# Kernel tuning notes

Measured on AMD Instinct MI355X. Metric: run time of the kernel, lower is better.

The kernel has to match this reference:

```python
import jax, jax.numpy as jnp
import numpy as np
from jax import lax

DIVISOR = 2.0


def setup_inputs() -> dict:
    key = jax.random.key(0)
    k1, k2, k3, k4 = jax.random.split(key, 4)
    x = jax.random.normal(k1, (128, 8, 32, 32, 32), dtype=jnp.float32)
    conv_weight = jax.random.normal(k2, (16, 8, 3, 3, 3), dtype=jnp.float32) * 0.1
    conv_bias = jax.random.normal(k3, (16,), dtype=jnp.float32) * 0.1
    bias = jax.random.normal(k4, (16, 1, 1, 1), dtype=jnp.float32) * 0.1
    return {"x": x, "conv_weight": conv_weight, "conv_bias": conv_bias, "bias": bias}


def reference(x, conv_weight, conv_bias, bias):
    # Conv3d, stride 1, no padding: [B,8,32,32,32] -> [B,16,30,30,30]
    y = lax.conv_general_dilated(
        x, conv_weight,
        window_strides=(1, 1, 1), padding='VALID',
        dimension_numbers=('NCDHW', 'OIDHW', 'NCDHW'))
    y = y + conv_bias[None, :, None, None, None]
    # divide by scalar divisor
    y = y / DIVISOR
    # MaxPool3d kernel=stride=2: [B,16,30,30,30] -> [B,16,15,15,15]
    y = lax.reduce_window(
        y, -jnp.inf, lax.max,
        window_dimensions=(1, 1, 2, 2, 2),
        window_strides=(1, 1, 2, 2, 2),
        padding='VALID')
    # AdaptiveAvgPool3d((1,1,1)): global mean over D,H,W -> [B,16,1,1,1]
    y = jnp.mean(y, axis=(2, 3, 4), keepdims=True)
    # bias add (bias shape [16,1,1,1] broadcasts over batch)
    y = y + bias
    # sum over channel dim (dim=1) -> [B,1,1,1]
    return jnp.sum(y, axis=1)
```

## Files before the change

kernel.cpp:

```cpp
#include <hip/hip_runtime.h>


using short8 = __attribute__((ext_vector_type(8))) short;
using f32x4  = __attribute__((ext_vector_type(4))) float;

__device__ __forceinline__ unsigned short f2bf_rn(float f) {
  unsigned u = __float_as_uint(f);
  return (unsigned short)((u + 0x7FFFu + ((u >> 16) & 1u)) >> 16);
}

__global__ __launch_bounds__(256) void prep_w(const float* __restrict__ cw,
                                              short* __restrict__ Bp) {
  int i = threadIdx.x + blockIdx.x * 256;
  if (i >= 576) return;
  int g = i >> 6, l = i & 63;
  int co = l & 15, kw = l >> 4;
  int kd = g / 3, kh = g % 3;
  short8 o;
#pragma unroll
  for (int j = 0; j < 8; ++j) {
    float v = (kw < 3) ? cw[(co * 8 + j) * 27 + kd * 9 + kh * 3 + kw] : 0.0f;
    o[j] = (short)f2bf_rn(v);
  }
  *(short8*)(Bp + (size_t)i * 8) = o;
}

__global__ __launch_bounds__(256, 4) void conv_mfma(const float* __restrict__ x,
                                                    const short* __restrict__ Bp,
                                                    float* __restrict__ partial) {
  __shared__ __align__(16) char lds[6 * 3072];
  __shared__ float red[4];

  const int bid = blockIdx.x;
  const int swz = (bid & 7) * 128 + (bid >> 3);
  const int b = swz >> 3, q = swz & 7;
  const int t = threadIdx.x, lane = t & 63, wv = t >> 6;
  const int nrows = (q == 7) ? 4 : 6;
  const int row0 = 4 * q;
  const int nsite = 2 * nrows * 16;
  const float* xb = x + (size_t)b * 262144;

  const bool sact = t < nsite;
  const int ss = sact ? t : 0;
  const int spl = ss / (nrows * 16);
  const int rem = ss - spl * (nrows * 16);
  const int sr = rem >> 4, swg = rem & 15;
  const float* gsite = xb + (row0 + sr) * 32 + swg * 2;

  auto issue = [&](int dpair, float2* v) {
    if (!sact) return;
    const float* gp = gsite + (dpair + spl) * 1024;
#pragma unroll
    for (int ci = 0; ci < 8; ++ci) v[ci] = *(const float2*)(gp + ci * 32768);
  };
  auto writeSlab = [&](int dpair, const float2* v) {
    if (!sact) return;
    const int d = dpair + spl;
    char* sb = lds + (d % 6) * 3072 + sr * 512;
#pragma unroll
    for (int wi = 0; wi < 2; ++wi) {
      const int w = swg * 2 + wi;
      uint4 o;
      o.x = __builtin_amdgcn_perm(__float_as_uint(((const float*)&v[1])[wi]),
                                  __float_as_uint(((const float*)&v[0])[wi]), 0x07060302u);
      o.y = __builtin_amdgcn_perm(__float_as_uint(((const float*)&v[3])[wi]),
                                  __float_as_uint(((const float*)&v[2])[wi]), 0x07060302u);
      o.z = __builtin_amdgcn_perm(__float_as_uint(((const float*)&v[5])[wi]),
                                  __float_as_uint(((const float*)&v[4])[wi]), 0x07060302u);
      o.w = __builtin_amdgcn_perm(__float_as_uint(((const float*)&v[7])[wi]),
                                  __float_as_uint(((const float*)&v[6])[wi]), 0x07060302u);
      *(uint4*)(sb + ((w * 16) ^ (((w >> 3) & 3) << 4))) = o;
    }
  };

  short8 Bw[9];
#pragma unroll
  for (int g = 0; g < 9; ++g)
    Bw[g] = *(const short8*)(Bp + ((size_t)g * 64 + lane) * 8);

  const int m = lane & 15, tg = lane >> 4;
  const int w0 = m + tg;
  int w1 = m + 16 + tg; if (w1 > 31) w1 = 31;
  const int wb0 = (w0 * 16) ^ (((w0 >> 3) & 3) << 4);
  const int wb1 = (w1 * 16) ^ (((w1 >> 3) & 3) << 4);

  const bool docomp = (q < 7) || (wv < 2);
  const int op = (q < 7) ? (wv >> 1) : 0;
  const int c  = (q < 7) ? (wv & 1) : wv;
  const int wbase = (c ? wb1 : wb0) + (2 * op) * 512;

  {
    float2 va[8], vb[8];
    issue(0, va); issue(2, vb);
    writeSlab(0, va); writeSlab(2, vb);
  }
  __syncthreads();

  float sum = 0.0f;
  for (int pd = 0; pd < 15; ++pd) {
    const bool more = (pd < 14);
    float2 va[8];
    if (more) issue(2 * pd + 4, va);

    if (docomp) {
      const char* sb0 = lds + ((2 * pd)     % 6) * 3072 + wbase;
      const char* sb1 = lds + ((2 * pd + 1) % 6) * 3072 + wbase;
      const char* sb2 = lds + ((2 * pd + 2) % 6) * 3072 + wbase;
      const char* sb3 = lds + ((2 * pd + 3) % 6) * 3072 + wbase;
      const char* sbp[4] = {sb0, sb1, sb2, sb3};
      f32x4 cc[2][2] = {};
#pragma unroll
      for (int p = 0; p < 4; ++p) {
#pragma unroll
        for (int rr = 0; rr < 4; ++rr) {
          const short8 a = *(const short8*)(sbp[p] + rr * 512);
          if (p < 3 && rr < 3)
            cc[0][0] = __builtin_amdgcn_mfma_f32_16x16x32_bf16(a, Bw[p * 3 + rr], cc[0][0], 0, 0, 0);
          if (p < 3 && rr > 0)
            cc[0][1] = __builtin_amdgcn_mfma_f32_16x16x32_bf16(a, Bw[p * 3 + rr - 1], cc[0][1], 0, 0, 0);
          if (p > 0 && rr < 3)
            cc[1][0] = __builtin_amdgcn_mfma_f32_16x16x32_bf16(a, Bw[(p - 1) * 3 + rr], cc[1][0], 0, 0, 0);
          if (p > 0 && rr > 0)
            cc[1][1] = __builtin_amdgcn_mfma_f32_16x16x32_bf16(a, Bw[(p - 1) * 3 + rr - 1], cc[1][1], 0, 0, 0);
        }
      }
#pragma unroll
      for (int p2 = 0; p2 < 2; ++p2) {
        float v = fmaxf(fmaxf(fmaxf(cc[0][0][2 * p2], cc[0][0][2 * p2 + 1]),
                              fmaxf(cc[0][1][2 * p2], cc[0][1][2 * p2 + 1])),
                        fmaxf(fmaxf(cc[1][0][2 * p2], cc[1][0][2 * p2 + 1]),
                              fmaxf(cc[1][1][2 * p2], cc[1][1][2 * p2 + 1])));
        const bool inval = (c == 1) && (tg == 3) && (p2 == 1);
        sum += inval ? 0.0f : v;
      }
    }

    if (more) writeSlab(2 * pd + 4, va);
    __syncthreads();
  }

#pragma unroll
  for (int off = 32; off; off >>= 1) sum += __shfl_down(sum, off);
  if (lane == 0) red[wv] = sum;
  __syncthreads();
  if (t == 0) partial[b * 8 + q] = red[0] + red[1] + red[2] + red[3];
}

__global__ __launch_bounds__(128) void finalize(const float* __restrict__ partial,
                                                const float* __restrict__ cb,
                                                const float* __restrict__ bias,
                                                float* __restrict__ out) {
  const int b = threadIdx.x;
  float k = 0.0f;
#pragma unroll
  for (int c = 0; c < 16; ++c) k += cb[c] * 0.5f + bias[c];
  float s = 0.0f;
#pragma unroll
  for (int q = 0; q < 8; ++q) s += partial[b * 8 + q];
  out[b] = s * (1.0f / 6750.0f) + k;
}

extern "C" void kernel_launch(void* const* d_in, const int* in_sizes, int n_in,
                              void* d_out, int out_size, void* d_ws, size_t ws_size,
                              hipStream_t stream) {
  const float* x    = (const float*)d_in[0];
  const float* cw   = (const float*)d_in[1];
  const float* cb   = (const float*)d_in[2];
  const float* bias = (const float*)d_in[3];
  float* out = (float*)d_out;

  short* Bp      = (short*)d_ws;
  float* partial = (float*)((char*)d_ws + 32768);

  prep_w<<<3, 256, 0, stream>>>(cw, Bp);
  conv_mfma<<<1024, 256, 0, stream>>>(x, Bp, partial);
  finalize<<<1, 128, 0, stream>>>(partial, cb, bias, out);
}
```

Measured before the change: 42.33 us.

## Fuse weight prep into conv kernel and deepen global-load pipeline

Drops the separate weight-preparation launch: each wave now converts its conv weights to bf16 fragments straight from global memory inside the conv kernel. The slab pipeline becomes two register buffers that are issued two iterations ahead, and writes into LDS now happen before compute instead of after it. The modulo slot indexing is replaced by rolling counters, and MFMA sections raise wave priority. This removes one kernel launch and hides more global-load latency, at the cost of redundant per-block weight loads and conversions plus extra register pressure.

```diff
diff --git a/kernel.cpp b/kernel.cpp
--- a/kernel.cpp
+++ b/kernel.cpp
@@ -9,25 +9,9 @@
   return (unsigned short)((u + 0x7FFFu + ((u >> 16) & 1u)) >> 16);
 }
 
-__global__ __launch_bounds__(256) void prep_w(const float* __restrict__ cw,
-                                              short* __restrict__ Bp) {
-  int i = threadIdx.x + blockIdx.x * 256;
-  if (i >= 576) return;
-  int g = i >> 6, l = i & 63;
-  int co = l & 15, kw = l >> 4;
-  int kd = g / 3, kh = g % 3;
-  short8 o;
-#pragma unroll
-  for (int j = 0; j < 8; ++j) {
-    float v = (kw < 3) ? cw[(co * 8 + j) * 27 + kd * 9 + kh * 3 + kw] : 0.0f;
-    o[j] = (short)f2bf_rn(v);
-  }
-  *(short8*)(Bp + (size_t)i * 8) = o;
-}
-
-__global__ __launch_bounds__(256, 4) void conv_mfma(const float* __restrict__ x,
-                                                    const short* __restrict__ Bp,
-                                                    float* __restrict__ partial) {
+__global__ __launch_bounds__(256, 4) void conv_fused(
+    const float* __restrict__ x, const float* __restrict__ cw,
+    float* __restrict__ partial) {
   __shared__ __align__(16) char lds[6 * 3072];
   __shared__ float red[4];
 
@@ -37,26 +21,40 @@
   const int t = threadIdx.x, lane = t & 63, wv = t >> 6;
   const int nrows = (q == 7) ? 4 : 6;
   const int row0 = 4 * q;
-  const int nsite = 2 * nrows * 16;
+  const int sites = nrows * 16;
   const float* xb = x + (size_t)b * 262144;
 
-  const bool sact = t < nsite;
-  const int ss = sact ? t : 0;
-  const int spl = ss / (nrows * 16);
-  const int rem = ss - spl * (nrows * 16);
-  const int sr = rem >> 4, swg = rem & 15;
+  const int m = lane & 15, tg = lane >> 4;
+
+  short8 Bw[9];
+#pragma unroll
+  for (int g = 0; g < 9; ++g) {
+    const int tgs = (tg < 3) ? tg : 0;
+    const float* wp = cw + (g / 3) * 9 + (g % 3) * 3 + tgs;
+    short8 o;
+#pragma unroll
+    for (int j = 0; j < 8; ++j) {
+      const float v = wp[(m * 8 + j) * 27];
+      o[j] = (tg < 3) ? (short)f2bf_rn(v) : (short)0;
+    }
+    Bw[g] = o;
+  }
+
+  const bool sact = t < 2 * sites;
+  const int spl = (t >= sites) ? 1 : 0;
+  const int ss = sact ? (t - spl * sites) : 0;
+  const int sr = ss >> 4, swg = ss & 15;
   const float* gsite = xb + (row0 + sr) * 32 + swg * 2;
 
-  auto issue = [&](int dpair, float2* v) {
+  auto issueB = [&](int pb, float2* v) {
     if (!sact) return;
-    const float* gp = gsite + (dpair + spl) * 1024;
+    const float* gp = gsite + (pb + spl) * 1024;
 #pragma unroll
     for (int ci = 0; ci < 8; ++ci) v[ci] = *(const float2*)(gp + ci * 32768);
   };
-  auto writeSlab = [&](int dpair, const float2* v) {
+  auto writeB = [&](int ws0, const float2* v) {
     if (!sact) return;
-    const int d = dpair + spl;
-    char* sb = lds + (d % 6) * 3072 + sr * 512;
+    char* sb = lds + (ws0 + spl) * 3072 + sr * 512;
 #pragma unroll
     for (int wi = 0; wi < 2; ++wi) {
       const int w = swg * 2 + wi;
@@ -73,12 +71,6 @@
     }
   };
 
-  short8 Bw[9];
-#pragma unroll
-  for (int g = 0; g < 9; ++g)
-    Bw[g] = *(const short8*)(Bp + ((size_t)g * 64 + lane) * 8);
-
-  const int m = lane & 15, tg = lane >> 4;
   const int w0 = m + tg;
   int w1 = m + 16 + tg; if (w1 > 31) w1 = 31;
   const int wb0 = (w0 * 16) ^ (((w0 >> 3) & 3) << 4);
@@ -89,26 +81,34 @@
   const int c  = (q < 7) ? (wv & 1) : wv;
   const int wbase = (c ? wb1 : wb0) + (2 * op) * 512;
 
-  {
-    float2 va[8], vb[8];
-    issue(0, va); issue(2, vb);
-    writeSlab(0, va); writeSlab(2, vb);
-  }
+  float2 bufA[8], bufB[8];
+  issueB(0, bufA);
+  issueB(2, bufB);
+  writeB(0, bufA);
+  issueB(4, bufA);
+  writeB(2, bufB);
+  issueB(6, bufB);
   __syncthreads();
 
   float sum = 0.0f;
+  int rs0 = 0;
+  int wsl = 4;
+  int wpl = 8;
   for (int pd = 0; pd < 15; ++pd) {
-    const bool more = (pd < 14);
-    float2 va[8];
-    if (more) issue(2 * pd + 4, va);
+    if (pd <= 13) {
+      float2* buf = (pd & 1) ? bufB : bufA;
+      writeB(wsl, buf);
+      if (pd <= 11) issueB(wpl, buf);
+    }
 
     if (docomp) {
-      const char* sb0 = lds + ((2 * pd)     % 6) * 3072 + wbase;
-      const char* sb1 = lds + ((2 * pd + 1) % 6) * 3072 + wbase;
-      const char* sb2 = lds + ((2 * pd + 2) % 6) * 3072 + wbase;
-      const char* sb3 = lds + ((2 * pd + 3) % 6) * 3072 + wbase;
-      const char* sbp[4] = {sb0, sb1, sb2, sb3};
+      int sl1 = rs0 + 1;
+      int sl2 = rs0 + 2; if (sl2 >= 6) sl2 -= 6;
+      int sl3 = rs0 + 3; if (sl3 >= 6) sl3 -= 6;
+      const char* sbp[4] = {lds + rs0 * 3072 + wbase, lds + sl1 * 3072 + wbase,
+                            lds + sl2 * 3072 + wbase, lds + sl3 * 3072 + wbase};
       f32x4 cc[2][2] = {};
+      __builtin_amdgcn_s_setprio(1);
 #pragma unroll
       for (int p = 0; p < 4; ++p) {
 #pragma unroll
@@ -124,6 +124,7 @@
             cc[1][1] = __builtin_amdgcn_mfma_f32_16x16x32_bf16(a, Bw[(p - 1) * 3 + rr - 1], cc[1][1], 0, 0, 0);
         }
       }
+      __builtin_amdgcn_s_setprio(0);
 #pragma unroll
       for (int p2 = 0; p2 < 2; ++p2) {
         float v = fmaxf(fmaxf(fmaxf(cc[0][0][2 * p2], cc[0][0][2 * p2 + 1]),
@@ -135,8 +136,10 @@
       }
     }
 
-    if (more) writeSlab(2 * pd + 4, va);
     __syncthreads();
+    rs0 += 2; if (rs0 >= 6) rs0 -= 6;
+    wsl += 2; if (wsl >= 6) wsl -= 6;
+    wpl += 2;
   }
 
 #pragma unroll
@@ -168,11 +171,8 @@
   const float* cb   = (const float*)d_in[2];
   const float* bias = (const float*)d_in[3];
   float* out = (float*)d_out;
+  float* partial = (float*)d_ws;
 
-  short* Bp      = (short*)d_ws;
-  float* partial = (float*)((char*)d_ws + 32768);
-
-  prep_w<<<3, 256, 0, stream>>>(cw, Bp);
-  conv_mfma<<<1024, 256, 0, stream>>>(x, Bp, partial);
+  conv_fused<<<1024, 256, 0, stream>>>(x, cw, partial);
   finalize<<<1, 128, 0, stream>>>(partial, cb, bias, out);
 }
```

Measured after the change: 65.89 us. 55.7% more time.

## Split depth range across two blocks per tile to double grid size

Applied to the files above, without the earlier changes.

Each (batch, row-strip) work item is now split along the depth axis into two halves, giving 2048 blocks instead of 1024. The occupancy hint rises to 8 blocks per SM, and ring-buffer slot indices are tracked incrementally instead of with modulo. The goal is more parallelism and a shorter serial depth loop per block, which should hide latency better. The cost is that each half reloads the two overlapping halo depth slices and runs an extra prologue, and finalize now sums 16 partials instead of 8.

```diff
diff --git a/kernel.cpp b/kernel.cpp
--- a/kernel.cpp
+++ b/kernel.cpp
@@ -25,38 +25,40 @@
   *(short8*)(Bp + (size_t)i * 8) = o;
 }
 
-__global__ __launch_bounds__(256, 4) void conv_mfma(const float* __restrict__ x,
+__global__ __launch_bounds__(256, 8) void conv_mfma(const float* __restrict__ x,
                                                     const short* __restrict__ Bp,
                                                     float* __restrict__ partial) {
   __shared__ __align__(16) char lds[6 * 3072];
   __shared__ float red[4];
 
   const int bid = blockIdx.x;
-  const int swz = (bid & 7) * 128 + (bid >> 3);
-  const int b = swz >> 3, q = swz & 7;
+  const int swz = (bid & 7) * 256 + (bid >> 3);
+  const int b = swz >> 4;
+  const int q = (swz >> 1) & 7;
+  const int half = swz & 1;
   const int t = threadIdx.x, lane = t & 63, wv = t >> 6;
   const int nrows = (q == 7) ? 4 : 6;
   const int row0 = 4 * q;
-  const int nsite = 2 * nrows * 16;
+  const int sites = nrows * 16;
+  const int pbase = half ? 16 : 0;
+  const int nsteps = half ? 7 : 8;
   const float* xb = x + (size_t)b * 262144;
 
-  const bool sact = t < nsite;
-  const int ss = sact ? t : 0;
-  const int spl = ss / (nrows * 16);
-  const int rem = ss - spl * (nrows * 16);
-  const int sr = rem >> 4, swg = rem & 15;
+  const bool sact = t < 2 * sites;
+  const int spl = (t >= sites) ? 1 : 0;
+  const int ss = sact ? (t - spl * sites) : 0;
+  const int sr = ss >> 4, swg = ss & 15;
   const float* gsite = xb + (row0 + sr) * 32 + swg * 2;
 
-  auto issue = [&](int dpair, float2* v) {
+  auto issueB = [&](int lp, float2* v) {
     if (!sact) return;
-    const float* gp = gsite + (dpair + spl) * 1024;
+    const float* gp = gsite + (pbase + lp + spl) * 1024;
 #pragma unroll
     for (int ci = 0; ci < 8; ++ci) v[ci] = *(const float2*)(gp + ci * 32768);
   };
-  auto writeSlab = [&](int dpair, const float2* v) {
+  auto writeB = [&](int lp, const float2* v) {
     if (!sact) return;
-    const int d = dpair + spl;
-    char* sb = lds + (d % 6) * 3072 + sr * 512;
+    char* sb = lds + ((lp + spl) % 6) * 3072 + sr * 512;
 #pragma unroll
     for (int wi = 0; wi < 2; ++wi) {
       const int w = swg * 2 + wi;
@@ -91,23 +93,26 @@
 
   {
     float2 va[8], vb[8];
-    issue(0, va); issue(2, vb);
-    writeSlab(0, va); writeSlab(2, vb);
+    issueB(0, va);
+    issueB(2, vb);
+    writeB(0, va);
+    writeB(2, vb);
   }
   __syncthreads();
 
   float sum = 0.0f;
-  for (int pd = 0; pd < 15; ++pd) {
-    const bool more = (pd < 14);
+  int rs0 = 0;
+  for (int st = 0; st < nsteps; ++st) {
+    const bool more = (st < nsteps - 1);
     float2 va[8];
-    if (more) issue(2 * pd + 4, va);
+    if (more) issueB(2 * st + 4, va);
 
     if (docomp) {
-      const char* sb0 = lds + ((2 * pd)     % 6) * 3072 + wbase;
-      const char* sb1 = lds + ((2 * pd + 1) % 6) * 3072 + wbase;
-      const char* sb2 = lds + ((2 * pd + 2) % 6) * 3072 + wbase;
-      const char* sb3 = lds + ((2 * pd + 3) % 6) * 3072 + wbase;
-      const char* sbp[4] = {sb0, sb1, sb2, sb3};
+      int sl1 = rs0 + 1;
+      int sl2 = rs0 + 2; if (sl2 >= 6) sl2 -= 6;
+      int sl3 = rs0 + 3; if (sl3 >= 6) sl3 -= 6;
+      const char* sbp[4] = {lds + rs0 * 3072 + wbase, lds + sl1 * 3072 + wbase,
+                            lds + sl2 * 3072 + wbase, lds + sl3 * 3072 + wbase};
       f32x4 cc[2][2] = {};
 #pragma unroll
       for (int p = 0; p < 4; ++p) {
@@ -135,15 +140,16 @@
       }
     }
 
-    if (more) writeSlab(2 * pd + 4, va);
+    if (more) writeB(2 * st + 4, va);
     __syncthreads();
+    rs0 += 2; if (rs0 >= 6) rs0 -= 6;
   }
 
 #pragma unroll
   for (int off = 32; off; off >>= 1) sum += __shfl_down(sum, off);
   if (lane == 0) red[wv] = sum;
   __syncthreads();
-  if (t == 0) partial[b * 8 + q] = red[0] + red[1] + red[2] + red[3];
+  if (t == 0) partial[b * 16 + q * 2 + half] = red[0] + red[1] + red[2] + red[3];
 }
 
 __global__ __launch_bounds__(128) void finalize(const float* __restrict__ partial,
@@ -156,7 +162,7 @@
   for (int c = 0; c < 16; ++c) k += cb[c] * 0.5f + bias[c];
   float s = 0.0f;
 #pragma unroll
-  for (int q = 0; q < 8; ++q) s += partial[b * 8 + q];
+  for (int i = 0; i < 16; ++i) s += partial[b * 16 + i];
   out[b] = s * (1.0f / 6750.0f) + k;
 }
 
@@ -173,6 +179,6 @@
   float* partial = (float*)((char*)d_ws + 32768);
 
   prep_w<<<3, 256, 0, stream>>>(cw, Bp);
-  conv_mfma<<<1024, 256, 0, stream>>>(x, Bp, partial);
+  conv_mfma<<<2048, 256, 0, stream>>>(x, Bp, partial);
   finalize<<<1, 128, 0, stream>>>(partial, cb, bias, out);
 }
```

Measured after the change: 136.8 us. 223% more time.

## Process two depth pairs per barrier with a deeper LDS ring buffer

Applied to the files above, without the earlier changes.

The LDS ring grows from 6 to 10 depth slabs, and each loop iteration now loads and writes two depth-pair slabs while computing two output depth pairs. That halves the number of __syncthreads barriers and keeps more global loads in flight. For the q==7 blocks the row-split waves are repurposed to work on different depth pairs, so all four waves do useful work instead of two. The cost is more LDS per block, which may reduce occupancy, and more complex slot indexing.

```diff
diff --git a/kernel.cpp b/kernel.cpp
--- a/kernel.cpp
+++ b/kernel.cpp
@@ -28,7 +28,7 @@
 __global__ __launch_bounds__(256, 4) void conv_mfma(const float* __restrict__ x,
                                                     const short* __restrict__ Bp,
                                                     float* __restrict__ partial) {
-  __shared__ __align__(16) char lds[6 * 3072];
+  __shared__ __align__(16) char lds[10 * 3072];
   __shared__ float red[4];
 
   const int bid = blockIdx.x;
@@ -37,26 +37,25 @@
   const int t = threadIdx.x, lane = t & 63, wv = t >> 6;
   const int nrows = (q == 7) ? 4 : 6;
   const int row0 = 4 * q;
-  const int nsite = 2 * nrows * 16;
+  const int sites = nrows * 16;
   const float* xb = x + (size_t)b * 262144;
 
-  const bool sact = t < nsite;
-  const int ss = sact ? t : 0;
-  const int spl = ss / (nrows * 16);
-  const int rem = ss - spl * (nrows * 16);
-  const int sr = rem >> 4, swg = rem & 15;
+  const bool sact = t < 2 * sites;
+  const int spl = (t >= sites) ? 1 : 0;
+  const int ss = sact ? (t - spl * sites) : 0;
+  const int sr = ss >> 4, swg = ss & 15;
   const float* gsite = xb + (row0 + sr) * 32 + swg * 2;
 
-  auto issue = [&](int dpair, float2* v) {
+  auto issueB = [&](int pb, float2* v) {
     if (!sact) return;
-    const float* gp = gsite + (dpair + spl) * 1024;
+    const float* gp = gsite + (pb + spl) * 1024;
 #pragma unroll
     for (int ci = 0; ci < 8; ++ci) v[ci] = *(const float2*)(gp + ci * 32768);
   };
-  auto writeSlab = [&](int dpair, const float2* v) {
+  auto writeS = [&](int sl0, const float2* v) {
     if (!sact) return;
-    const int d = dpair + spl;
-    char* sb = lds + (d % 6) * 3072 + sr * 512;
+    int slot = sl0 + spl; if (slot >= 10) slot -= 10;
+    char* sb = lds + slot * 3072 + sr * 512;
 #pragma unroll
     for (int wi = 0; wi < 2; ++wi) {
       const int w = swg * 2 + wi;
@@ -84,60 +83,81 @@
   const int wb0 = (w0 * 16) ^ (((w0 >> 3) & 3) << 4);
   const int wb1 = (w1 * 16) ^ (((w1 >> 3) & 3) << 4);
 
-  const bool docomp = (q < 7) || (wv < 2);
-  const int op = (q < 7) ? (wv >> 1) : 0;
-  const int c  = (q < 7) ? (wv & 1) : wv;
-  const int wbase = (c ? wb1 : wb0) + (2 * op) * 512;
+  const int op = wv >> 1, c = wv & 1;
+  const int rowoff = (q < 7) ? (2 * op) : 0;
+  const int wbase = (c ? wb1 : wb0) + rowoff * 512;
+  const int rot = (q < 7) ? op : 0;
+  const int dp7 = op;
+
+  float sum = 0.0f;
+  auto compute = [&](int rs) {
+    int s0 = rs;      if (s0 >= 10) s0 -= 10;
+    int s1 = rs + 1;  if (s1 >= 10) s1 -= 10;
+    int s2 = rs + 2;  if (s2 >= 10) s2 -= 10;
+    int s3 = rs + 3;  if (s3 >= 10) s3 -= 10;
+    const char* sbp[4] = {lds + s0 * 3072 + wbase, lds + s1 * 3072 + wbase,
+                          lds + s2 * 3072 + wbase, lds + s3 * 3072 + wbase};
+    f32x4 cc[2][2] = {};
+#pragma unroll
+    for (int p = 0; p < 4; ++p) {
+#pragma unroll
+      for (int rr = 0; rr < 4; ++rr) {
+        const short8 a = *(const short8*)(sbp[p] + rr * 512);
+        if (p < 3 && rr < 3)
+          cc[0][0] = __builtin_amdgcn_mfma_f32_16x16x32_bf16(a, Bw[p * 3 + rr], cc[0][0], 0, 0, 0);
+        if (p < 3 && rr > 0)
+          cc[0][1] = __builtin_amdgcn_mfma_f32_16x16x32_bf16(a, Bw[p * 3 + rr - 1], cc[0][1], 0, 0, 0);
+        if (p > 0 && rr < 3)
+          cc[1][0] = __builtin_amdgcn_mfma_f32_16x16x32_bf16(a, Bw[(p - 1) * 3 + rr], cc[1][0], 0, 0, 0);
+        if (p > 0 && rr > 0)
+          cc[1][1] = __builtin_amdgcn_mfma_f32_16x16x32_bf16(a, Bw[(p - 1) * 3 + rr - 1], cc[1][1], 0, 0, 0);
+      }
+    }
+#pragma unroll
+    for (int p2 = 0; p2 < 2; ++p2) {
+      float v = fmaxf(fmaxf(fmaxf(cc[0][0][2 * p2], cc[0][0][2 * p2 + 1]),
+                            fmaxf(cc[0][1][2 * p2], cc[0][1][2 * p2 + 1])),
+                      fmaxf(fmaxf(cc[1][0][2 * p2], cc[1][0][2 * p2 + 1]),
+                            fmaxf(cc[1][1][2 * p2], cc[1][1][2 * p2 + 1])));
+      const bool inval = (c == 1) && (tg == 3) && (p2 == 1);
+      sum += inval ? 0.0f : v;
+    }
+  };
 
   {
     float2 va[8], vb[8];
-    issue(0, va); issue(2, vb);
-    writeSlab(0, va); writeSlab(2, vb);
+    issueB(0, va);
+    issueB(2, vb);
+    writeS(0, va);
+    issueB(4, va);
+    writeS(2, vb);
+    writeS(4, va);
   }
   __syncthreads();
 
-  float sum = 0.0f;
-  for (int pd = 0; pd < 15; ++pd) {
-    const bool more = (pd < 14);
-    float2 va[8];
-    if (more) issue(2 * pd + 4, va);
+  int r0 = 0;
+#pragma unroll 1
+  for (int k = 0; k < 7; ++k) {
+    const bool haveB = (k < 6);
+    float2 va[8], vb[8];
+    issueB(4 * k + 6, va);
 
-    if (docomp) {
-      const char* sb0 = lds + ((2 * pd)     % 6) * 3072 + wbase;
-      const char* sb1 = lds + ((2 * pd + 1) % 6) * 3072 + wbase;
-      const char* sb2 = lds + ((2 * pd + 2) % 6) * 3072 + wbase;
-      const char* sb3 = lds + ((2 * pd + 3) % 6) * 3072 + wbase;
-      const char* sbp[4] = {sb0, sb1, sb2, sb3};
-      f32x4 cc[2][2] = {};
-#pragma unroll
-      for (int p = 0; p < 4; ++p) {
-#pragma unroll
-        for (int rr = 0; rr < 4; ++rr) {
-          const short8 a = *(const short8*)(sbp[p] + rr * 512);
-          if (p < 3 && rr < 3)
-            cc[0][0] = __builtin_amdgcn_mfma_f32_16x16x32_bf16(a, Bw[p * 3 + rr], cc[0][0], 0, 0, 0);
-          if (p < 3 && rr > 0)
-            cc[0][1] = __builtin_amdgcn_mfma_f32_16x16x32_bf16(a, Bw[p * 3 + rr - 1], cc[0][1], 0, 0, 0);
-          if (p > 0 && rr < 3)
-            cc[1][0] = __builtin_amdgcn_mfma_f32_16x16x32_bf16(a, Bw[(p - 1) * 3 + rr], cc[1][0], 0, 0, 0);
-          if (p > 0 && rr > 0)
-            cc[1][1] = __builtin_amdgcn_mfma_f32_16x16x32_bf16(a, Bw[(p - 1) * 3 + rr - 1], cc[1][1], 0, 0, 0);
-        }
-      }
-#pragma unroll
-      for (int p2 = 0; p2 < 2; ++p2) {
-        float v = fmaxf(fmaxf(fmaxf(cc[0][0][2 * p2], cc[0][0][2 * p2 + 1]),
-                              fmaxf(cc[0][1][2 * p2], cc[0][1][2 * p2 + 1])),
-                        fmaxf(fmaxf(cc[1][0][2 * p2], cc[1][0][2 * p2 + 1]),
-                              fmaxf(cc[1][1][2 * p2], cc[1][1][2 * p2 + 1])));
-        const bool inval = (c == 1) && (tg == 3) && (p2 == 1);
-        sum += inval ? 0.0f : v;
-      }
-    }
+    if (q < 7) compute(r0 + 2 * rot);
+    else       compute(r0 + 2 * dp7);
 
-    if (more) writeSlab(2 * pd + 4, va);
+    writeS(r0 + 6, va);
+    if (haveB) issueB(4 * k + 8, vb);
+
+    if (q < 7) compute(r0 + 2 * (1 - rot));
+
+    if (haveB) writeS(r0 + 8, vb);
+
     __syncthreads();
+    r0 += 4; if (r0 >= 10) r0 -= 10;
   }
+
+  if (q < 7) compute(r0);
+  else if (dp7 == 0) compute(r0);
 
 #pragma unroll
   for (int off = 32; off; off >>= 1) sum += __shfl_down(sum, off);
```

New measurement: 52.16 us. 1.23x slower.
